# Kernel optimization log

Hardware: AMD Instinct MI355X
Metric: run time of the kernel (lower is better)

Reference implementation:

```python
import jax, jax.numpy as jnp
from jax import lax
import numpy as np

KSIZE = 3
NUM_GAB = 16
NUM_IMAP = 16
BATCH = 4096


def gabor_bank(theta, sigma, gamma, lambd, psi, ksize=KSIZE):
    # vectorized version of the original triple Python loop
    offs = jnp.arange(ksize, dtype=theta.dtype) - 1.0  # (x-1), (y-1) in source
    xg, yg = jnp.meshgrid(offs, offs, indexing='ij')   # [K,K]
    c = jnp.cos(theta)[:, None, None]
    s = jnp.sin(theta)[:, None, None]
    xt = xg * c + yg * s        # [F,K,K]
    yt = -xg * s + yg * c
    sx = sigma[:, None, None]
    sy = (sigma / gamma)[:, None, None]
    env = jnp.exp(-0.5 * (xt ** 2 / sx ** 2 + yt ** 2 / sy ** 2))
    car = jnp.cos(2.0 * jnp.pi * xt / lambd[:, None, None] + psi[:, None, None])
    return env * car  # [F,K,K]


def maxpool2(x):
    return lax.reduce_window(x, -jnp.inf, lax.max, (1, 1, 2, 2), (1, 1, 2, 2), 'VALID')


def setup_inputs() -> dict:
    key = jax.random.key(0)
    ks = jax.random.split(key, 12)
    x = jax.random.normal(ks[0], (BATCH, 1, 28, 28), dtype=jnp.float32)
    theta = jax.random.uniform(ks[1], (NUM_GAB,), minval=0.0, maxval=180.0)
    sigma = jax.random.uniform(ks[2], (NUM_GAB,), minval=0.0, maxval=360.0)
    gamma = jax.random.uniform(ks[3], (NUM_GAB,), minval=0.0, maxval=1.0)
    lambd = jax.random.uniform(ks[4], (NUM_GAB,), minval=2.0, maxval=10.0)
    psi = jnp.zeros((NUM_GAB,), dtype=jnp.float32)
    conv2_w = jax.random.normal(ks[5], (64, 32, 3, 3), dtype=jnp.float32) * 0.05
    conv2_b = jnp.zeros((64,), dtype=jnp.float32)
    fc1_w = jax.random.normal(ks[6], (128, 3136), dtype=jnp.float32) * 0.02
    fc1_b = jnp.zeros((128,), dtype=jnp.float32)
    fc2_w = jax.random.normal(ks[7], (10, 128), dtype=jnp.float32) * 0.1
    fc2_b = jnp.zeros((10,), dtype=jnp.float32)
    return dict(x=x, theta=theta, sigma=sigma, gamma=gamma, lambd=lambd, psi=psi,
                conv2_w=conv2_w, conv2_b=conv2_b, fc1_w=fc1_w, fc1_b=fc1_b,
                fc2_w=fc2_w, fc2_b=fc2_b)


def reference(x, theta, sigma, gamma, lambd, psi, conv2_w, conv2_b, fc1_w, fc1_b, fc2_w, fc2_b):
    kern = gabor_bank(theta, sigma, gamma, lambd, psi)          # [16,3,3]
    imaps = jnp.zeros((NUM_IMAP, KSIZE, KSIZE), dtype=x.dtype).at[:, 1, 1].set(1.0)
    w1 = jnp.concatenate([kern, imaps], axis=0)[:, None]         # [32,1,3,3]
    dn = ('NCHW', 'OIHW', 'NCHW')
    out = lax.conv_general_dilated(x, w1, (1, 1), [(1, 1), (1, 1)], dimension_numbers=dn)
    out = maxpool2(jax.nn.relu(out))                             # [B,32,14,14]
    out = lax.conv_general_dilated(out, conv2_w, (1, 1), [(1, 1), (1, 1)], dimension_numbers=dn)
    out = maxpool2(jax.nn.relu(out + conv2_b[None, :, None, None]))  # [B,64,7,7]
    out = out.reshape(out.shape[0], -1)                          # [B,3136]
    out = jax.nn.relu(out @ fc1_w.T + fc1_b)                     # dropout = identity (eval)
    out = out @ fc2_w.T + fc2_b                                  # [B,10]
    return out
```

## Files before the change

### kernel.cpp

```cpp
#include <hip/hip_runtime.h>
#include <hip/hip_bf16.h>

#define BATCH 4096

typedef unsigned short u16;
typedef _Float16 half4 __attribute__((ext_vector_type(4)));
typedef _Float16 half8 __attribute__((ext_vector_type(8)));
typedef short bs8 __attribute__((ext_vector_type(8)));
typedef float floatx4 __attribute__((ext_vector_type(4)));
typedef float floatx16 __attribute__((ext_vector_type(16)));

__device__ inline u16 f2bf(float f) {
    union { float f; unsigned int i; } u;
    u.f = f;
    unsigned int lsb = (u.i >> 16) & 1u;
    unsigned int r = u.i + 0x7fffu + lsb;
    if ((u.i & 0x7f800000u) == 0x7f800000u) r = u.i;
    return (u16)(r >> 16);
}

__global__ __launch_bounds__(256) void prep_kernel(
        const float* __restrict__ theta, const float* __restrict__ sigma,
        const float* __restrict__ gamma, const float* __restrict__ lambd,
        const float* __restrict__ psi, const float* __restrict__ conv2_w,
        const float* __restrict__ fc1_w, _Float16* __restrict__ w1h,
        _Float16* __restrict__ w2h, u16* __restrict__ wbf) {
    int id = blockIdx.x * 256 + threadIdx.x;
    if (id < 512) {
        int g = id >> 4, t = id & 15;
        float v = 0.0f;
        if (t < 9) {
            int i = t / 3, j = t % 3;
            float xg = (float)i - 1.0f;
            float yg = (float)j - 1.0f;
            if (g < 16) {
                float th = theta[g];
                float c = cosf(th), s = sinf(th);
                float xt = xg * c + yg * s;
                float yt = -xg * s + yg * c;
                float sx = sigma[g];
                float sy = sx / gamma[g];
                float env = expf(-0.5f *
                                 (xt * xt / (sx * sx) + yt * yt / (sy * sy)));
                float car =
                    cosf(6.28318530717958647692f * xt / lambd[g] + psi[g]);
                v = env * car;
            } else {
                v = (t == 4) ? 1.0f : 0.0f;
            }
        }
        w1h[id] = (_Float16)v;
    } else if (id < 512 + 18432) {
        int t2 = id - 512;
        int tap = t2 / 2048, rem = t2 % 2048;
        int oc = rem / 32, ic = rem % 32;
        w2h[t2] = (_Float16)conv2_w[(oc * 32 + ic) * 9 + tap];
    } else {
        int t3 = id - 512 - 18432;
        int nrow = t3 / 3200, kp = t3 % 3200;
        int oc = kp / 50, pl = kp % 50;
        wbf[t3] =
            pl < 49 ? f2bf(fc1_w[(size_t)nrow * 3136 + oc * 49 + pl]) : 0;
    }
}

__global__ __launch_bounds__(256) void fused_conv_kernel(
        const float* __restrict__ x, const _Float16* __restrict__ w1h,
        const _Float16* __restrict__ w2h, const float* __restrict__ conv2_b,
        u16* __restrict__ a2) {
    __shared__ _Float16 img16[30][32];
    __shared__ __align__(16) _Float16 a1s[16][16][40];
    __shared__ u16 out2[64 * 50];

    int n = blockIdx.x;
    int tid = threadIdx.x;
    int lane = tid & 63;
    int w = tid >> 6;
    int l16 = lane & 15;
    int quad = lane >> 4;
    int l32 = lane & 31;
    int h = lane >> 5;

    int nt = w & 1;
    int mt0 = w >> 1;
    int oc = nt * 32 + l32;
    half8 bE[9], bO[9];
    const _Float16* bp = w2h + (size_t)oc * 32 + h * 8;
#pragma unroll
    for (int t = 0; t < 9; ++t) {
        bE[t] = *(const half8*)(bp + t * 2048);
        bO[t] = *(const half8*)(bp + t * 2048 + 16);
    }
    float bias = conv2_b[oc];

    for (int i = tid; i < 120; i += 256) ((int4*)&img16[0][0])[i] = int4{0,0,0,0};
    for (int i = tid; i < 1280; i += 256) ((int4*)&a1s[0][0][0])[i] = int4{0,0,0,0};
    for (int i = tid; i < 400; i += 256) ((int4*)&out2[0])[i] = int4{0,0,0,0};
    __syncthreads();

    const float* xim = x + (size_t)n * 784;
    for (int i = tid; i < 784; i += 256)
        img16[i / 28 + 1][i % 28 + 1] = (_Float16)xim[i];
    __syncthreads();

    half4 b1a = *(const half4*)&w1h[l16 * 16 + quad * 4];
    half4 b1b = *(const half4*)&w1h[(16 + l16) * 16 + quad * 4];
    int t0 = quad * 4;
    int off0 = (t0 / 3) * 32 + (t0 % 3);
    int off1 = ((t0 + 1) / 3) * 32 + ((t0 + 1) % 3);
    int off2 = ((t0 + 2) / 3) * 32 + ((t0 + 2) % 3);
    int off3 = ((t0 + 3) / 3) * 32 + ((t0 + 3) % 3);
    bool v0ok = t0 < 9, v1ok = t0 + 1 < 9, v2ok = t0 + 2 < 9, v3ok = t0 + 3 < 9;
    int sy = (l16 & 3) >> 1, sx = l16 & 1;

    int pool0 = w * 4 + (l16 >> 2);
    int a14 = pool0 >= 14 ? 1 : 0;
    int b14 = pool0 - 14 * a14;
    int pl0 = w * 4 + quad;
    int pa = pl0 >= 14 ? 1 : 0;
    int pb = pl0 - 14 * pa;

    for (int mt = w; mt < 49; mt += 4) {
        const _Float16* p = &img16[2 * a14 + sy][2 * b14 + sx];
        half4 av;
        av[0] = v0ok ? p[off0] : (_Float16)0.0f;
        av[1] = v1ok ? p[off1] : (_Float16)0.0f;
        av[2] = v2ok ? p[off2] : (_Float16)0.0f;
        av[3] = v3ok ? p[off3] : (_Float16)0.0f;
        floatx4 c0 = {0.f, 0.f, 0.f, 0.f};
        floatx4 c1 = {0.f, 0.f, 0.f, 0.f};
        c0 = __builtin_amdgcn_mfma_f32_16x16x16f16(av, b1a, c0, 0, 0, 0);
        c1 = __builtin_amdgcn_mfma_f32_16x16x16f16(av, b1b, c1, 0, 0, 0);
        float m0 = fmaxf(fmaxf(c0[0], c0[1]), fmaxf(c0[2], c0[3]));
        float m1 = fmaxf(fmaxf(c1[0], c1[1]), fmaxf(c1[2], c1[3]));
        a1s[1 + pa][1 + pb][l16] = (_Float16)fmaxf(m0, 0.0f);
        a1s[1 + pa][1 + pb][16 + l16] = (_Float16)fmaxf(m1, 0.0f);
        a14 += 1; b14 += 2;
        if (b14 >= 14) { b14 -= 14; a14 += 1; }
        pa += 1; pb += 2;
        if (pb >= 14) { pb -= 14; pa += 1; }
    }
    __syncthreads();

    for (int mt = mt0; mt < 7; mt += 2) {
        int pool = mt * 8 + (l32 >> 2);
        int sub = l32 & 3;
        int pc = pool < 49 ? pool : 48;
        int y = 2 * (pc / 7) + (sub >> 1);
        int xq = 2 * (pc % 7) + (sub & 1);
        const _Float16* ap = &a1s[y][xq][h * 8];
        floatx16 accE = {};
        floatx16 accO = {};
#pragma unroll
        for (int t = 0; t < 9; ++t) {
            int ao = ((t / 3) * 16 + (t % 3)) * 40;
            half8 avE = *(const half8*)(ap + ao);
            half8 avO = *(const half8*)(ap + ao + 16);
            accE = __builtin_amdgcn_mfma_f32_32x32x16_f16(avE, bE[t], accE,
                                                          0, 0, 0);
            accO = __builtin_amdgcn_mfma_f32_32x32x16_f16(avO, bO[t], accO,
                                                          0, 0, 0);
        }
#pragma unroll
        for (int rg = 0; rg < 4; ++rg) {
            int pl = mt * 8 + 2 * rg + h;
            if (pl < 49) {
                float v0 = accE[rg * 4 + 0] + accO[rg * 4 + 0];
                float v1 = accE[rg * 4 + 1] + accO[rg * 4 + 1];
                float v2 = accE[rg * 4 + 2] + accO[rg * 4 + 2];
                float v3 = accE[rg * 4 + 3] + accO[rg * 4 + 3];
                float mx = fmaxf(fmaxf(v0, v1), fmaxf(v2, v3));
                out2[oc * 50 + pl] = f2bf(fmaxf(mx + bias, 0.0f));
            }
        }
    }
    __syncthreads();

    uint2* dst = (uint2*)(a2 + (size_t)n * 3200);
    const uint2* src = (const uint2*)out2;
    for (int i = tid; i < 800; i += 256) dst[i] = src[i];
}

__global__ __launch_bounds__(1024) void fc_kernel(
        const u16* __restrict__ A, const u16* __restrict__ Wbf,
        const float* __restrict__ fc1_b, const float* __restrict__ fc2_w,
        const float* __restrict__ fc2_b, float* __restrict__ out) {
    __shared__ float Hs[8][16][132];
    int tid = threadIdx.x;
    int lane = tid & 63;
    int w = tid >> 6;
    int l16 = lane & 15;
    int quad = lane >> 4;
    int kq = w >> 1;
    int nh = w & 1;
    int m0 = blockIdx.x * 16;

    const u16* aptr = A + (size_t)(m0 + l16) * 3200 + quad * 8;
    const u16* b0 = Wbf + (size_t)(nh * 64 + l16) * 3200 + quad * 8;
    const u16* b1 = b0 + 16 * 3200;
    const u16* b2 = b0 + 32 * 3200;
    const u16* b3 = b0 + 48 * 3200;

    floatx4 ac0 = {0.f, 0.f, 0.f, 0.f};
    floatx4 ac1 = {0.f, 0.f, 0.f, 0.f};
    floatx4 ac2 = {0.f, 0.f, 0.f, 0.f};
    floatx4 ac3 = {0.f, 0.f, 0.f, 0.f};
#pragma unroll 4
    for (int s = kq; s < 100; s += 8) {
        int k0 = s * 32;
        bs8 av = *(const bs8*)(aptr + k0);
        bs8 bv0 = *(const bs8*)(b0 + k0);
        bs8 bv1 = *(const bs8*)(b1 + k0);
        bs8 bv2 = *(const bs8*)(b2 + k0);
        bs8 bv3 = *(const bs8*)(b3 + k0);
        ac0 = __builtin_amdgcn_mfma_f32_16x16x32_bf16(av, bv0, ac0, 0, 0, 0);
        ac1 = __builtin_amdgcn_mfma_f32_16x16x32_bf16(av, bv1, ac1, 0, 0, 0);
        ac2 = __builtin_amdgcn_mfma_f32_16x16x32_bf16(av, bv2, ac2, 0, 0, 0);
        ac3 = __builtin_amdgcn_mfma_f32_16x16x32_bf16(av, bv3, ac3, 0, 0, 0);
    }
    int nb = nh * 64 + l16;
#pragma unroll
    for (int r = 0; r < 4; ++r) {
        int mr = quad * 4 + r;
        Hs[kq][mr][nb] = ac0[r];
        Hs[kq][mr][nb + 16] = ac1[r];
        Hs[kq][mr][nb + 32] = ac2[r];
        Hs[kq][mr][nb + 48] = ac3[r];
    }
    __syncthreads();

    for (int i = tid; i < 2048; i += 1024) {
        int m = i >> 7, k = i & 127;
        float s = Hs[0][m][k] + Hs[1][m][k] + Hs[2][m][k] + Hs[3][m][k] +
                  Hs[4][m][k] + Hs[5][m][k] + Hs[6][m][k] + Hs[7][m][k];
        Hs[0][m][k] = s;
    }
    __syncthreads();

    if (tid < 160) {
        int m = tid / 10, j = tid % 10;
        const float* wr = fc2_w + j * 128;
        float acc = fc2_b[j];
#pragma unroll 16
        for (int k = 0; k < 128; ++k)
            acc += fmaxf(Hs[0][m][k] + fc1_b[k], 0.0f) * wr[k];
        out[(size_t)(m0 + m) * 10 + j] = acc;
    }
}

extern "C" void kernel_launch(void* const* d_in, const int* in_sizes, int n_in,
                              void* d_out, int out_size, void* d_ws,
                              size_t ws_size, hipStream_t stream) {
    const float* x       = (const float*)d_in[0];
    const float* theta   = (const float*)d_in[1];
    const float* sigma   = (const float*)d_in[2];
    const float* gamma   = (const float*)d_in[3];
    const float* lambd   = (const float*)d_in[4];
    const float* psi     = (const float*)d_in[5];
    const float* conv2_w = (const float*)d_in[6];
    const float* conv2_b = (const float*)d_in[7];
    const float* fc1_w   = (const float*)d_in[8];
    const float* fc1_b   = (const float*)d_in[9];
    const float* fc2_w   = (const float*)d_in[10];
    const float* fc2_b   = (const float*)d_in[11];
    float* out = (float*)d_out;

    char* ws = (char*)d_ws;
    u16* a2 = (u16*)ws;
    _Float16* w1h = (_Float16*)(ws + 26214400ull);
    _Float16* w2h = (_Float16*)(ws + 26215424ull);
    u16* wbf = (u16*)(ws + 26252288ull);

    prep_kernel<<<1674, 256, 0, stream>>>(theta, sigma, gamma, lambd, psi,
                                          conv2_w, fc1_w, w1h, w2h, wbf);
    fused_conv_kernel<<<BATCH, 256, 0, stream>>>(x, w1h, w2h, conv2_b, a2);
    fc_kernel<<<BATCH / 16, 1024, 0, stream>>>(a2, wbf, fc1_b, fc2_w, fc2_b,
                                               out);
}
```

Before: 168.8 us.

## Switch conv2 to 16x16x32 MFMA tiles covering all 64 channels per wave

Conv2 previously used 32x32x16 MFMAs with even/odd K-halves, each wave handling 32 output channels and a 32-row M tile. Now each wave handles a 16-row M tile across all 64 output channels using four 16x16x32 MFMAs per tap. This drops the extra accumulator sum and lets the 2x2 pool run inside a lane's four accumulator values. It also replaces the conv1 bounds-check selects with clamped offsets, relying on the zero-padded tap weights. The cost is more B-fragment registers per wave (36 half8 vs 18).

```diff
diff --git a/kernel.cpp b/kernel.cpp
--- a/kernel.cpp
+++ b/kernel.cpp
@@ -8,7 +8,6 @@
 typedef _Float16 half8 __attribute__((ext_vector_type(8)));
 typedef short bs8 __attribute__((ext_vector_type(8)));
 typedef float floatx4 __attribute__((ext_vector_type(4)));
-typedef float floatx16 __attribute__((ext_vector_type(16)));
 
 __device__ inline u16 f2bf(float f) {
     union { float f; unsigned int i; } u;
@@ -78,20 +77,17 @@
     int w = tid >> 6;
     int l16 = lane & 15;
     int quad = lane >> 4;
-    int l32 = lane & 31;
-    int h = lane >> 5;
-
-    int nt = w & 1;
-    int mt0 = w >> 1;
-    int oc = nt * 32 + l32;
-    half8 bE[9], bO[9];
-    const _Float16* bp = w2h + (size_t)oc * 32 + h * 8;
-#pragma unroll
-    for (int t = 0; t < 9; ++t) {
-        bE[t] = *(const half8*)(bp + t * 2048);
-        bO[t] = *(const half8*)(bp + t * 2048 + 16);
-    }
-    float bias = conv2_b[oc];
+
+    half8 bf[9][4];
+#pragma unroll
+    for (int t = 0; t < 9; ++t)
+#pragma unroll
+        for (int nt = 0; nt < 4; ++nt)
+            bf[t][nt] = *(const half8*)&w2h[(t * 64 + nt * 16 + l16) * 32 +
+                                            quad * 8];
+    float bias[4];
+#pragma unroll
+    for (int nt = 0; nt < 4; ++nt) bias[nt] = conv2_b[nt * 16 + l16];
 
     for (int i = tid; i < 120; i += 256) ((int4*)&img16[0][0])[i] = int4{0,0,0,0};
     for (int i = tid; i < 1280; i += 256) ((int4*)&a1s[0][0][0])[i] = int4{0,0,0,0};
@@ -106,11 +102,12 @@
     half4 b1a = *(const half4*)&w1h[l16 * 16 + quad * 4];
     half4 b1b = *(const half4*)&w1h[(16 + l16) * 16 + quad * 4];
     int t0 = quad * 4;
-    int off0 = (t0 / 3) * 32 + (t0 % 3);
-    int off1 = ((t0 + 1) / 3) * 32 + ((t0 + 1) % 3);
-    int off2 = ((t0 + 2) / 3) * 32 + ((t0 + 2) % 3);
-    int off3 = ((t0 + 3) / 3) * 32 + ((t0 + 3) % 3);
-    bool v0ok = t0 < 9, v1ok = t0 + 1 < 9, v2ok = t0 + 2 < 9, v3ok = t0 + 3 < 9;
+    int u0 = t0 < 9 ? t0 : 8, u1 = t0 + 1 < 9 ? t0 + 1 : 8;
+    int u2 = t0 + 2 < 9 ? t0 + 2 : 8, u3 = t0 + 3 < 9 ? t0 + 3 : 8;
+    int off0 = (u0 / 3) * 32 + (u0 % 3);
+    int off1 = (u1 / 3) * 32 + (u1 % 3);
+    int off2 = (u2 / 3) * 32 + (u2 % 3);
+    int off3 = (u3 / 3) * 32 + (u3 % 3);
     int sy = (l16 & 3) >> 1, sx = l16 & 1;
 
     int pool0 = w * 4 + (l16 >> 2);
@@ -123,10 +120,10 @@
     for (int mt = w; mt < 49; mt += 4) {
         const _Float16* p = &img16[2 * a14 + sy][2 * b14 + sx];
         half4 av;
-        av[0] = v0ok ? p[off0] : (_Float16)0.0f;
-        av[1] = v1ok ? p[off1] : (_Float16)0.0f;
-        av[2] = v2ok ? p[off2] : (_Float16)0.0f;
-        av[3] = v3ok ? p[off3] : (_Float16)0.0f;
+        av[0] = p[off0];
+        av[1] = p[off1];
+        av[2] = p[off2];
+        av[3] = p[off3];
         floatx4 c0 = {0.f, 0.f, 0.f, 0.f};
         floatx4 c1 = {0.f, 0.f, 0.f, 0.f};
         c0 = __builtin_amdgcn_mfma_f32_16x16x16f16(av, b1a, c0, 0, 0, 0);
@@ -142,36 +139,38 @@
     }
     __syncthreads();
 
-    for (int mt = mt0; mt < 7; mt += 2) {
-        int pool = mt * 8 + (l32 >> 2);
-        int sub = l32 & 3;
+    u16* o2 = &out2[l16 * 50];
+    for (int mt = w; mt < 13; mt += 4) {
+        int m = mt * 16 + l16;
+        int pool = m >> 2;
+        int sub = m & 3;
         int pc = pool < 49 ? pool : 48;
         int y = 2 * (pc / 7) + (sub >> 1);
         int xq = 2 * (pc % 7) + (sub & 1);
-        const _Float16* ap = &a1s[y][xq][h * 8];
-        floatx16 accE = {};
-        floatx16 accO = {};
+        const _Float16* ap = &a1s[y][xq][quad * 8];
+        floatx4 a0 = {0.f, 0.f, 0.f, 0.f};
+        floatx4 a1 = {0.f, 0.f, 0.f, 0.f};
+        floatx4 a2c = {0.f, 0.f, 0.f, 0.f};
+        floatx4 a3 = {0.f, 0.f, 0.f, 0.f};
 #pragma unroll
         for (int t = 0; t < 9; ++t) {
             int ao = ((t / 3) * 16 + (t % 3)) * 40;
-            half8 avE = *(const half8*)(ap + ao);
-            half8 avO = *(const half8*)(ap + ao + 16);
-            accE = __builtin_amdgcn_mfma_f32_32x32x16_f16(avE, bE[t], accE,
-                                                          0, 0, 0);
-            accO = __builtin_amdgcn_mfma_f32_32x32x16_f16(avO, bO[t], accO,
-                                                          0, 0, 0);
+            half8 av = *(const half8*)(ap + ao);
+            a0 = __builtin_amdgcn_mfma_f32_16x16x32_f16(av, bf[t][0], a0, 0, 0, 0);
+            a1 = __builtin_amdgcn_mfma_f32_16x16x32_f16(av, bf[t][1], a1, 0, 0, 0);
+            a2c = __builtin_amdgcn_mfma_f32_16x16x32_f16(av, bf[t][2], a2c, 0, 0, 0);
+            a3 = __builtin_amdgcn_mfma_f32_16x16x32_f16(av, bf[t][3], a3, 0, 0, 0);
         }
-#pragma unroll
-        for (int rg = 0; rg < 4; ++rg) {
-            int pl = mt * 8 + 2 * rg + h;
-            if (pl < 49) {
-                float v0 = accE[rg * 4 + 0] + accO[rg * 4 + 0];
-                float v1 = accE[rg * 4 + 1] + accO[rg * 4 + 1];
-                float v2 = accE[rg * 4 + 2] + accO[rg * 4 + 2];
-                float v3 = accE[rg * 4 + 3] + accO[rg * 4 + 3];
-                float mx = fmaxf(fmaxf(v0, v1), fmaxf(v2, v3));
-                out2[oc * 50 + pl] = f2bf(fmaxf(mx + bias, 0.0f));
-            }
+        int pl = mt * 4 + quad;
+        if (pl < 49) {
+            float m0 = fmaxf(fmaxf(a0[0], a0[1]), fmaxf(a0[2], a0[3]));
+            float m1 = fmaxf(fmaxf(a1[0], a1[1]), fmaxf(a1[2], a1[3]));
+            float m2 = fmaxf(fmaxf(a2c[0], a2c[1]), fmaxf(a2c[2], a2c[3]));
+            float m3 = fmaxf(fmaxf(a3[0], a3[1]), fmaxf(a3[2], a3[3]));
+            o2[pl] = f2bf(fmaxf(m0 + bias[0], 0.0f));
+            o2[16 * 50 + pl] = f2bf(fmaxf(m1 + bias[1], 0.0f));
+            o2[32 * 50 + pl] = f2bf(fmaxf(m2 + bias[2], 0.0f));
+            o2[48 * 50 + pl] = f2bf(fmaxf(m3 + bias[3], 0.0f));
         }
     }
     __syncthreads();
```

Measured after the change: 192.3 us. 13.9% more time.
